# Optimization experiments

Hardware: AMD Instinct MI355X
Metric: run time of the kernel (lower is better)

Reference implementation:

```python
import jax, jax.numpy as jnp
import numpy as np

POOLED_H = 7
POOLED_W = 7
SAMPLING_RATIO = 2


def setup_inputs() -> dict:
    key = jax.random.key(0)
    k1, k2, k3, k4 = jax.random.split(key, 4)
    B, C, H, W = 2, 256, 192, 192
    N = 1024
    stride = 16
    img_h, img_w = H * stride, W * stride
    feature = jax.random.normal(k1, (B, C, H, W), dtype=jnp.float32)
    # well-formed rois: (batch_idx, x1, y1, x2, y2) in image coordinates
    bidx = jax.random.randint(k2, (N, 1), 0, B).astype(jnp.float32)
    p1 = jax.random.uniform(k3, (N, 2), minval=0.0, maxval=0.7)
    wh = jax.random.uniform(k4, (N, 2), minval=0.02, maxval=0.3)
    x1y1 = p1 * jnp.array([img_w, img_h], jnp.float32)
    x2y2 = jnp.minimum(x1y1 + wh * jnp.array([img_w, img_h], jnp.float32),
                       jnp.array([img_w - 1.0, img_h - 1.0], jnp.float32))
    rois = jnp.concatenate([bidx, x1y1[:, :1], x1y1[:, 1:], x2y2[:, :1], x2y2[:, 1:]], axis=1)
    return {"rois": rois, "feature": feature, "stride": stride}


def _roi_align(feature, rois, pooled_h, pooled_w, spatial_scale, ratio):
    B, C, H, W = feature.shape
    N = rois.shape[0]
    b = rois[:, 0].astype(jnp.int32)                     # [N]
    x1 = rois[:, 1] * spatial_scale
    y1 = rois[:, 2] * spatial_scale
    x2 = rois[:, 3] * spatial_scale
    y2 = rois[:, 4] * spatial_scale
    roi_w = jnp.maximum(x2 - x1, 1.0)                    # classic (non-aligned) RoIAlign
    roi_h = jnp.maximum(y2 - y1, 1.0)
    bin_w = roi_w / pooled_w
    bin_h = roi_h / pooled_h

    Sy, Sx = pooled_h * ratio, pooled_w * ratio
    iy = (jnp.arange(Sy, dtype=feature.dtype) + 0.5) / ratio  # in units of bin_h
    ix = (jnp.arange(Sx, dtype=feature.dtype) + 0.5) / ratio
    y = y1[:, None] + iy[None, :] * bin_h[:, None]       # [N, Sy]
    x = x1[:, None] + ix[None, :] * bin_w[:, None]       # [N, Sx]

    def interp_axis(c, size):
        valid = (c > -1.0) & (c < size)
        cc = jnp.clip(c, 0.0, size - 1)
        lo = jnp.floor(cc).astype(jnp.int32)
        lo = jnp.minimum(lo, size - 1)
        hi = jnp.minimum(lo + 1, size - 1)
        frac = cc - lo.astype(c.dtype)
        return valid, lo, hi, frac

    vy, y0, y1i, fy = interp_axis(y, H)
    vx, x0, x1i, fx = interp_axis(x, W)

    hy, ly = (1.0 - fy), fy                              # [N, Sy]
    hx, lx = (1.0 - fx), fx                              # [N, Sx]

    bI = b[:, None, None]

    def gather(yi, xi):
        # -> [N, Sy, Sx, C]
        return feature[bI, :, yi[:, :, None], xi[:, None, :]]

    val = (hy[:, :, None] * hx[:, None, :])[..., None] * gather(y0, x0) \
        + (hy[:, :, None] * lx[:, None, :])[..., None] * gather(y0, x1i) \
        + (ly[:, :, None] * hx[:, None, :])[..., None] * gather(y1i, x0) \
        + (ly[:, :, None] * lx[:, None, :])[..., None] * gather(y1i, x1i)
    val = val * (vy[:, :, None] & vx[:, None, :])[..., None].astype(val.dtype)

    # average sampling grid within each bin
    out = val.reshape(N, pooled_h, ratio, pooled_w, ratio, C).mean(axis=(2, 4))
    return out.transpose(0, 3, 1, 2)                     # [N, C, pooled_h, pooled_w]


def reference(rois, feature, stride):
    rois = rois[:, :5].astype(feature.dtype)
    spatial_scale = 1.0 / stride
    return _roi_align(feature, rois, POOLED_H, POOLED_W, spatial_scale, SAMPLING_RATIO)
```

## Files before the change

### kernel.cpp

```cpp
#include <hip/hip_runtime.h>
#include <hip/hip_fp16.h>

#define POOLED 7
#define RATIO 2

constexpr int C_ = 256;
constexpr int H_ = 192;
constexpr int W_ = 192;
constexpr int P_ = H_ * W_;
constexpr int PP2 = POOLED * POOLED;

constexpr int TC = 32;
constexpr int TP = 128;
constexpr int TPAD = TP + 1;

__global__ __launch_bounds__(256)
void nchw_to_nhwc_h(const float* __restrict__ in, __half* __restrict__ outT) {
    __shared__ float tile[TC][TPAD];
    const int b  = blockIdx.z;
    const int p0 = blockIdx.x * TP;
    const int c0 = blockIdx.y * TC;
    const float* src = in   + (size_t)b * C_ * P_;
    __half*      dst = outT + (size_t)b * P_ * C_;

    const int t = threadIdx.x;

    #pragma unroll
    for (int k = 0; k < 4; ++k) {
        const int q  = t + 256 * k;
        const int c  = q >> 5;
        const int pv = q & 31;
        const float4 v = *(const float4*)&src[(size_t)(c0 + c) * P_ + p0 + 4 * pv];
        tile[c][4 * pv + 0] = v.x;
        tile[c][4 * pv + 1] = v.y;
        tile[c][4 * pv + 2] = v.z;
        tile[c][4 * pv + 3] = v.w;
    }
    __syncthreads();

    #pragma unroll
    for (int k = 0; k < 2; ++k) {
        const int q  = t + 256 * k;
        const int p  = q >> 2;
        const int c8 = (q & 3) * 8;
        union { __half h[8]; float4 f; } u;
        #pragma unroll
        for (int i = 0; i < 8; ++i) u.h[i] = __float2half(tile[c8 + i][p]);
        *(float4*)&dst[(size_t)(p0 + p) * C_ + c0 + c8] = u.f;
    }
}

__device__ inline float4 h4_to_f4(uint2 r) {
    const float2 a = __half22float2(*(const __half2*)&r.x);
    const float2 b = __half22float2(*(const __half2*)&r.y);
    return make_float4(a.x, a.y, b.x, b.y);
}

__global__ __launch_bounds__(512)
void roi_align_nhwc_h(const float* __restrict__ rois,
                      const __half* __restrict__ featT,
                      const int* __restrict__ stride_ptr,
                      float* __restrict__ out, int N) {
    __shared__ __half lds_out[PP2 * C_];

    const int n    = blockIdx.x;
    const int lane = threadIdx.x & 63;
    const int wave = threadIdx.x >> 6;

    const float scale = 1.0f / (float)stride_ptr[0];
    const float* r = rois + (size_t)n * 5;
    const int   b  = (int)r[0];
    const float x1 = r[1] * scale;
    const float y1 = r[2] * scale;
    const float x2 = r[3] * scale;
    const float y2 = r[4] * scale;
    const float bin_w = fmaxf(x2 - x1, 1.0f) * (1.0f / (float)POOLED);
    const float bin_h = fmaxf(y2 - y1, 1.0f) * (1.0f / (float)POOLED);

    const uint2* fbase = (const uint2*)featT + (size_t)b * P_ * (C_ / 4);
    const int cb = lane * 4;

    for (int bin = wave; bin < PP2; bin += 8) {
        const int ph = bin / POOLED;
        const int pw = bin - ph * POOLED;

        float4 acc = make_float4(0.f, 0.f, 0.f, 0.f);

        #pragma unroll
        for (int sy = 0; sy < RATIO; ++sy) {
            const float yy = y1 + ((float)(ph * RATIO + sy) + 0.5f) * (1.0f / RATIO) * bin_h;
            const bool  vy = (yy > -1.0f) && (yy < (float)H_);
            float cy = fminf(fmaxf(yy, 0.0f), (float)(H_ - 1));
            int   y0 = (int)floorf(cy);
            if (y0 > H_ - 1) y0 = H_ - 1;
            const int   y1i = min(y0 + 1, H_ - 1);
            const float fy  = cy - (float)y0;
            const float hy  = 1.0f - fy;

            #pragma unroll
            for (int sx = 0; sx < RATIO; ++sx) {
                const float xx = x1 + ((float)(pw * RATIO + sx) + 0.5f) * (1.0f / RATIO) * bin_w;
                const bool  vx = (xx > -1.0f) && (xx < (float)W_);
                if (!(vy && vx)) continue;
                float cx = fminf(fmaxf(xx, 0.0f), (float)(W_ - 1));
                int   x0 = (int)floorf(cx);
                if (x0 > W_ - 1) x0 = W_ - 1;
                const int   x1i = min(x0 + 1, W_ - 1);
                const float fx  = cx - (float)x0;
                const float hx  = 1.0f - fx;

                const float w00 = hy * hx, w01 = hy * fx, w10 = fy * hx, w11 = fy * fx;

                const float4 v00 = h4_to_f4(fbase[(size_t)(y0  * W_ + x0 ) * (C_ / 4) + lane]);
                const float4 v01 = h4_to_f4(fbase[(size_t)(y0  * W_ + x1i) * (C_ / 4) + lane]);
                const float4 v10 = h4_to_f4(fbase[(size_t)(y1i * W_ + x0 ) * (C_ / 4) + lane]);
                const float4 v11 = h4_to_f4(fbase[(size_t)(y1i * W_ + x1i) * (C_ / 4) + lane]);

                acc.x = fmaf(w00, v00.x, fmaf(w01, v01.x, fmaf(w10, v10.x, fmaf(w11, v11.x, acc.x))));
                acc.y = fmaf(w00, v00.y, fmaf(w01, v01.y, fmaf(w10, v10.y, fmaf(w11, v11.y, acc.y))));
                acc.z = fmaf(w00, v00.z, fmaf(w01, v01.z, fmaf(w10, v10.z, fmaf(w11, v11.z, acc.z))));
                acc.w = fmaf(w00, v00.w, fmaf(w01, v01.w, fmaf(w10, v10.w, fmaf(w11, v11.w, acc.w))));
            }
        }

        union { __half2 h2[2]; uint2 u; } pk;
        pk.h2[0] = __float22half2_rn(make_float2(acc.x * 0.25f, acc.y * 0.25f));
        pk.h2[1] = __float22half2_rn(make_float2(acc.z * 0.25f, acc.w * 0.25f));
        *(uint2*)&lds_out[bin * C_ + cb] = pk.u;
    }

    __syncthreads();

    float4* o4 = (float4*)(out + (size_t)n * (C_ * PP2));
    for (int i = threadIdx.x; i < (C_ * PP2) / 4; i += 512) {
        const int l0 = i * 4;
        float4 v;
        #pragma unroll
        for (int j = 0; j < 4; ++j) {
            const int l  = l0 + j;
            const int c  = l / PP2;
            const int bn = l - c * PP2;
            ((float*)&v)[j] = __half2float(lds_out[bn * C_ + c]);
        }
        o4[i] = v;
    }
}

__global__ __launch_bounds__(256)
void roi_align_kernel(const float* __restrict__ rois,
                      const float* __restrict__ feat,
                      const int* __restrict__ stride_ptr,
                      int B, int C, int H, int W, int N,
                      float* __restrict__ out) {
    const int total = N * C * POOLED * POOLED;
    int idx = blockIdx.x * blockDim.x + threadIdx.x;
    if (idx >= total) return;

    const float scale = 1.0f / (float)stride_ptr[0];

    int pw = idx % POOLED;
    int ph = (idx / POOLED) % POOLED;
    int c  = (idx / (POOLED * POOLED)) % C;
    int n  = idx / (POOLED * POOLED * C);

    const float* r = rois + (size_t)n * 5;
    int b = (int)r[0];
    float x1 = r[1] * scale;
    float y1 = r[2] * scale;
    float x2 = r[3] * scale;
    float y2 = r[4] * scale;
    float bin_w = fmaxf(x2 - x1, 1.0f) / (float)POOLED;
    float bin_h = fmaxf(y2 - y1, 1.0f) / (float)POOLED;

    const float* plane = feat + ((size_t)b * C + c) * (size_t)(H * W);

    float acc = 0.0f;
    #pragma unroll
    for (int sy = 0; sy < RATIO; ++sy) {
        float iy = ((float)(ph * RATIO + sy) + 0.5f) / (float)RATIO;
        float yy = y1 + iy * bin_h;
        bool vy = (yy > -1.0f) && (yy < (float)H);
        float cy = fminf(fmaxf(yy, 0.0f), (float)(H - 1));
        int y0 = (int)floorf(cy);
        if (y0 > H - 1) y0 = H - 1;
        int y1i = min(y0 + 1, H - 1);
        float fy = cy - (float)y0;
        float hy = 1.0f - fy;

        #pragma unroll
        for (int sx = 0; sx < RATIO; ++sx) {
            float ix = ((float)(pw * RATIO + sx) + 0.5f) / (float)RATIO;
            float xx = x1 + ix * bin_w;
            bool vx = (xx > -1.0f) && (xx < (float)W);
            if (!(vy && vx)) continue;
            float cx = fminf(fmaxf(xx, 0.0f), (float)(W - 1));
            int x0 = (int)floorf(cx);
            if (x0 > W - 1) x0 = W - 1;
            int x1i = min(x0 + 1, W - 1);
            float fx = cx - (float)x0;
            float hx = 1.0f - fx;

            float v00 = plane[y0  * W + x0 ];
            float v01 = plane[y0  * W + x1i];
            float v10 = plane[y1i * W + x0 ];
            float v11 = plane[y1i * W + x1i];

            acc += hy * hx * v00 + hy * fx * v01 + fy * hx * v10 + fy * fx * v11;
        }
    }

    out[idx] = acc * 0.25f;
}

extern "C" void kernel_launch(void* const* d_in, const int* in_sizes, int n_in,
                              void* d_out, int out_size, void* d_ws, size_t ws_size,
                              hipStream_t stream) {
    const float* rois = (const float*)d_in[0];
    const float* feat = (const float*)d_in[1];
    const int* stride_ptr = (const int*)d_in[2];

    const int N = in_sizes[0] / 5;
    const int B = in_sizes[1] / (C_ * P_);
    float* out = (float*)d_out;

    const size_t need = (size_t)B * P_ * C_ * sizeof(__half);
    if (ws_size >= need) {
        __half* featT = (__half*)d_ws;
        dim3 tgrid(P_ / TP, C_ / TC, B);
        nchw_to_nhwc_h<<<tgrid, 256, 0, stream>>>(feat, featT);

        roi_align_nhwc_h<<<N, 512, 0, stream>>>(rois, featT, stride_ptr, out, N);
    } else {
        const int total = N * C_ * POOLED * POOLED;
        const int block = 256;
        const int grid = (total + block - 1) / block;
        roi_align_kernel<<<grid, block, 0, stream>>>(rois, feat, stride_ptr,
                                                     B, C_, H_, W_, N, out);
    }
}
```

Measured before the change: 169.0 us.

## Precompute per-ROI sample coords in LDS, accumulate in half2, pad LDS stride

Each ROI block now computes its 14 y and 14 x sample coordinates, weights and validity flags once into LDS, so the per-bin bilinear setup is no longer recomputed by every wave. Accumulation switches from fp32 FMAs with half-to-float conversion to packed __hfma2 on half2, with the 0.25 averaging folded into the weights. The LDS output buffer gets a padded row stride to reduce bank conflicts in the transposed readout. Half-precision accumulation lowers accuracy and adds a barrier, while the kernel stays dominated by memory gathers and the transpose.

```diff
diff --git a/kernel.cpp b/kernel.cpp
--- a/kernel.cpp
+++ b/kernel.cpp
@@ -50,32 +50,51 @@
     }
 }
 
-__device__ inline float4 h4_to_f4(uint2 r) {
-    const float2 a = __half22float2(*(const __half2*)&r.x);
-    const float2 b = __half22float2(*(const __half2*)&r.y);
-    return make_float4(a.x, a.y, b.x, b.y);
-}
-
 __global__ __launch_bounds__(512)
 void roi_align_nhwc_h(const float* __restrict__ rois,
                       const __half* __restrict__ featT,
                       const int* __restrict__ stride_ptr,
                       float* __restrict__ out, int N) {
-    __shared__ __half lds_out[PP2 * C_];
+    constexpr int BSTRIDE = C_ + 2;
+    __shared__ __half lds_out[PP2 * BSTRIDE];
+    __shared__ int4 coord[28];
 
     const int n    = blockIdx.x;
-    const int lane = threadIdx.x & 63;
-    const int wave = threadIdx.x >> 6;
+    const int t    = threadIdx.x;
+    const int lane = t & 63;
+    const int wave = t >> 6;
 
     const float scale = 1.0f / (float)stride_ptr[0];
     const float* r = rois + (size_t)n * 5;
-    const int   b  = (int)r[0];
-    const float x1 = r[1] * scale;
-    const float y1 = r[2] * scale;
-    const float x2 = r[3] * scale;
-    const float y2 = r[4] * scale;
-    const float bin_w = fmaxf(x2 - x1, 1.0f) * (1.0f / (float)POOLED);
-    const float bin_h = fmaxf(y2 - y1, 1.0f) * (1.0f / (float)POOLED);
+    const int   b   = (int)r[0];
+    const float rx1 = r[1] * scale;
+    const float ry1 = r[2] * scale;
+    const float rx2 = r[3] * scale;
+    const float ry2 = r[4] * scale;
+    const float bin_w = fmaxf(rx2 - rx1, 1.0f) * (1.0f / (float)POOLED);
+    const float bin_h = fmaxf(ry2 - ry1, 1.0f) * (1.0f / (float)POOLED);
+
+    if (t < 28) {
+        const bool  isY   = t < 14;
+        const int   s     = isY ? t : t - 14;
+        const float start = isY ? ry1 : rx1;
+        const float bsz   = isY ? bin_h : bin_w;
+        const int   size  = isY ? H_ : W_;
+        const float cc0   = start + ((float)s + 0.5f) * 0.5f * bsz;
+        const bool  valid = (cc0 > -1.0f) && (cc0 < (float)size);
+        float cc = fminf(fmaxf(cc0, 0.0f), (float)(size - 1));
+        int lo = (int)floorf(cc);
+        if (lo > size - 1) lo = size - 1;
+        const int hi = min(lo + 1, size - 1);
+        const float frac = (cc - (float)lo) * 0.5f;
+        int4 e;
+        e.x = isY ? lo * W_ : lo;
+        e.y = isY ? hi * W_ : hi;
+        e.z = __float_as_int(frac);
+        e.w = valid ? 1 : 0;
+        coord[t] = e;
+    }
+    __syncthreads();
 
     const uint2* fbase = (const uint2*)featT + (size_t)b * P_ * (C_ / 4);
     const int cb = lane * 4;
@@ -84,55 +103,60 @@
         const int ph = bin / POOLED;
         const int pw = bin - ph * POOLED;
 
-        float4 acc = make_float4(0.f, 0.f, 0.f, 0.f);
+        const int4 cxA = coord[14 + 2 * pw];
+        const int4 cxB = coord[14 + 2 * pw + 1];
+
+        __half2 acc01 = __float2half2_rn(0.f);
+        __half2 acc23 = __float2half2_rn(0.f);
 
         #pragma unroll
         for (int sy = 0; sy < RATIO; ++sy) {
-            const float yy = y1 + ((float)(ph * RATIO + sy) + 0.5f) * (1.0f / RATIO) * bin_h;
-            const bool  vy = (yy > -1.0f) && (yy < (float)H_);
-            float cy = fminf(fmaxf(yy, 0.0f), (float)(H_ - 1));
-            int   y0 = (int)floorf(cy);
-            if (y0 > H_ - 1) y0 = H_ - 1;
-            const int   y1i = min(y0 + 1, H_ - 1);
-            const float fy  = cy - (float)y0;
-            const float hy  = 1.0f - fy;
+            const int4  cy = coord[2 * ph + sy];
+            const float fy = __int_as_float(cy.z);
+            const float hy = 0.5f - fy;
 
             #pragma unroll
             for (int sx = 0; sx < RATIO; ++sx) {
-                const float xx = x1 + ((float)(pw * RATIO + sx) + 0.5f) * (1.0f / RATIO) * bin_w;
-                const bool  vx = (xx > -1.0f) && (xx < (float)W_);
-                if (!(vy && vx)) continue;
-                float cx = fminf(fmaxf(xx, 0.0f), (float)(W_ - 1));
-                int   x0 = (int)floorf(cx);
-                if (x0 > W_ - 1) x0 = W_ - 1;
-                const int   x1i = min(x0 + 1, W_ - 1);
-                const float fx  = cx - (float)x0;
-                const float hx  = 1.0f - fx;
-
-                const float w00 = hy * hx, w01 = hy * fx, w10 = fy * hx, w11 = fy * fx;
-
-                const float4 v00 = h4_to_f4(fbase[(size_t)(y0  * W_ + x0 ) * (C_ / 4) + lane]);
-                const float4 v01 = h4_to_f4(fbase[(size_t)(y0  * W_ + x1i) * (C_ / 4) + lane]);
-                const float4 v10 = h4_to_f4(fbase[(size_t)(y1i * W_ + x0 ) * (C_ / 4) + lane]);
-                const float4 v11 = h4_to_f4(fbase[(size_t)(y1i * W_ + x1i) * (C_ / 4) + lane]);
-
-                acc.x = fmaf(w00, v00.x, fmaf(w01, v01.x, fmaf(w10, v10.x, fmaf(w11, v11.x, acc.x))));
-                acc.y = fmaf(w00, v00.y, fmaf(w01, v01.y, fmaf(w10, v10.y, fmaf(w11, v11.y, acc.y))));
-                acc.z = fmaf(w00, v00.z, fmaf(w01, v01.z, fmaf(w10, v10.z, fmaf(w11, v11.z, acc.z))));
-                acc.w = fmaf(w00, v00.w, fmaf(w01, v01.w, fmaf(w10, v10.w, fmaf(w11, v11.w, acc.w))));
+                const int4 cx = sx ? cxB : cxA;
+                if (!(cy.w & cx.w)) continue;
+                const float fx = __int_as_float(cx.z);
+                const float hx = 0.5f - fx;
+
+                const __half2 W00 = __float2half2_rn(hy * hx);
+                const __half2 W01 = __float2half2_rn(hy * fx);
+                const __half2 W10 = __float2half2_rn(fy * hx);
+                const __half2 W11 = __float2half2_rn(fy * fx);
+
+                const int p00 = cy.x + cx.x;
+                const int p01 = cy.x + cx.y;
+                const int p10 = cy.y + cx.x;
+                const int p11 = cy.y + cx.y;
+
+                const uint2 r00 = fbase[(size_t)p00 * (C_ / 4) + lane];
+                const uint2 r01 = fbase[(size_t)p01 * (C_ / 4) + lane];
+                const uint2 r10 = fbase[(size_t)p10 * (C_ / 4) + lane];
+                const uint2 r11 = fbase[(size_t)p11 * (C_ / 4) + lane];
+
+                acc01 = __hfma2(W00, *(const __half2*)&r00.x, acc01);
+                acc23 = __hfma2(W00, *(const __half2*)&r00.y, acc23);
+                acc01 = __hfma2(W01, *(const __half2*)&r01.x, acc01);
+                acc23 = __hfma2(W01, *(const __half2*)&r01.y, acc23);
+                acc01 = __hfma2(W10, *(const __half2*)&r10.x, acc01);
+                acc23 = __hfma2(W10, *(const __half2*)&r10.y, acc23);
+                acc01 = __hfma2(W11, *(const __half2*)&r11.x, acc01);
+                acc23 = __hfma2(W11, *(const __half2*)&r11.y, acc23);
             }
         }
 
-        union { __half2 h2[2]; uint2 u; } pk;
-        pk.h2[0] = __float22half2_rn(make_float2(acc.x * 0.25f, acc.y * 0.25f));
-        pk.h2[1] = __float22half2_rn(make_float2(acc.z * 0.25f, acc.w * 0.25f));
-        *(uint2*)&lds_out[bin * C_ + cb] = pk.u;
+        __half2* dst = (__half2*)&lds_out[bin * BSTRIDE + cb];
+        dst[0] = acc01;
+        dst[1] = acc23;
     }
 
     __syncthreads();
 
     float4* o4 = (float4*)(out + (size_t)n * (C_ * PP2));
-    for (int i = threadIdx.x; i < (C_ * PP2) / 4; i += 512) {
+    for (int i = t; i < (C_ * PP2) / 4; i += 512) {
         const int l0 = i * 4;
         float4 v;
         #pragma unroll
@@ -140,7 +164,7 @@
             const int l  = l0 + j;
             const int c  = l / PP2;
             const int bn = l - c * PP2;
-            ((float*)&v)[j] = __half2float(lds_out[bn * C_ + c]);
+            ((float*)&v)[j] = __half2float(lds_out[bn * BSTRIDE + c]);
         }
         o4[i] = v;
     }
```

After: 165.6 us. 1.02x faster.
